# Performance work log

Measured on AMD Instinct MI355X. Metric: run time of the kernel, lower is better.

The kernel has to match this reference:

```python
import jax, jax.numpy as jnp
import numpy as np

N, E, F, H, C = 50000, 800000, 602, 32, 41
BN_EPS = 1e-5


def _mlp(h, Wa, ba, Wb, bb):
    return jax.nn.relu(h @ Wa + ba) @ Wb + bb


def _bn(h, gamma, beta):
    # BatchNorm1d training mode: per-feature batch mean / biased variance
    m = jnp.mean(h, axis=0)
    v = jnp.var(h, axis=0)
    return (h - m) * jax.lax.rsqrt(v + BN_EPS) * gamma + beta


def _gin(x, row, col, Wa, ba, Wb, bb):
    # sum-aggregate neighbor features (SpMM via gather + segment_sum), eps=0
    agg = jax.ops.segment_sum(x[col], row, num_segments=x.shape[0])
    return _mlp(x + agg, Wa, ba, Wb, bb)


def setup_inputs() -> dict:
    key = jax.random.key(0)
    ks = jax.random.split(key, 16)
    s = 0.05
    inp = {
        "x": jax.random.normal(ks[0], (N, F), dtype=jnp.float32),
        "row": jax.random.randint(ks[1], (E,), 0, N),
        "col": jax.random.randint(ks[2], (E,), 0, N),
        # conv1 MLP
        "W1a": jax.random.normal(ks[3], (F, H), dtype=jnp.float32) * s,
        "b1a": jnp.zeros((H,), jnp.float32),
        "W1b": jax.random.normal(ks[4], (H, H), dtype=jnp.float32) * s,
        "b1b": jnp.zeros((H,), jnp.float32),
        "g1": jnp.ones((H,), jnp.float32),
        "be1": jnp.zeros((H,), jnp.float32),
        # conv2 MLP
        "W2a": jax.random.normal(ks[5], (H, H), dtype=jnp.float32) * s,
        "b2a": jnp.zeros((H,), jnp.float32),
        "W2b": jax.random.normal(ks[6], (H, H), dtype=jnp.float32) * s,
        "b2b": jnp.zeros((H,), jnp.float32),
        "g2": jnp.ones((H,), jnp.float32),
        "be2": jnp.zeros((H,), jnp.float32),
        # heads
        "Wf1": jax.random.normal(ks[7], (H, H), dtype=jnp.float32) * s,
        "bf1": jnp.zeros((H,), jnp.float32),
        "Wf2": jax.random.normal(ks[8], (H, C), dtype=jnp.float32) * s,
        "bf2": jnp.zeros((C,), jnp.float32),
    }
    return inp


def reference(x, row, col, W1a, b1a, W1b, b1b, g1, be1,
              W2a, b2a, W2b, b2b, g2, be2, Wf1, bf1, Wf2, bf2):
    h = _bn(_gin(x, row, col, W1a, b1a, W1b, b1b), g1, be1)
    h = _bn(_gin(h, row, col, W2a, b2a, W2b, b2b), g2, be2)
    h = jax.nn.relu(h @ Wf1 + bf1)
    return h @ Wf2 + bf2
```

## Files before the change

### kernel.cpp

```cpp
#include <hip/hip_runtime.h>
#include <hip/hip_bf16.h>

#define N_NODES 50000
#define F_IN    602
#define H_DIM   32
#define C_OUT   41
#define E_EDGES 800000
#define BN_EPS  1e-5f

typedef short bf16x8 __attribute__((ext_vector_type(8)));
typedef float f32x4  __attribute__((ext_vector_type(4)));

__device__ inline unsigned short f2bf(float f) {
  unsigned int u = __builtin_bit_cast(unsigned int, f);
  unsigned int r = (u + 0x7FFFu + ((u >> 16) & 1u)) >> 16;
  return (unsigned short)r;
}

__global__ __launch_bounds__(256) void k_gemm_mfma(
    const float* __restrict__ x, const float* __restrict__ W,
    float* __restrict__ p) {
  __shared__ unsigned short xh[64 * 40], xl[64 * 40];
  __shared__ unsigned short wh[32 * 40], wl[32 * 40];
  const int tid = threadIdx.x;
  const int wv = tid >> 6, ln = tid & 63;
  const int m = ln & 15, q = ln >> 4;
  const int r0 = blockIdx.x * 64;

  const int srow = tid >> 4, ks2 = tid & 15;
  const int wk = tid >> 3, c4 = tid & 7;

  float2 xr[4];
  float4 wr;

  auto prefetch = [&](int k0) {
    #pragma unroll
    for (int pp = 0; pp < 4; pp++) {
      int rr = r0 + srow + 16 * pp;
      int k = k0 + 2 * ks2;
      float2 v = {0.f, 0.f};
      if (rr < N_NODES && k <= F_IN - 2) v = *(const float2*)(x + (size_t)rr * F_IN + k);
      xr[pp] = v;
    }
    {
      int k = k0 + wk;
      float4 v = {0.f, 0.f, 0.f, 0.f};
      if (k < F_IN) v = *(const float4*)(W + (size_t)k * H_DIM + 4 * c4);
      wr = v;
    }
  };

  f32x4 acc0 = {0.f, 0.f, 0.f, 0.f};
  f32x4 acc1 = {0.f, 0.f, 0.f, 0.f};

  prefetch(0);

  unsigned int* xh32 = (unsigned int*)xh;
  unsigned int* xl32 = (unsigned int*)xl;

  for (int ch = 0; ch < 19; ch++) {
    __syncthreads();
    #pragma unroll
    for (int pp = 0; pp < 4; pp++) {
      int row = srow + 16 * pp;
      float2 v = xr[pp];
      unsigned short h0 = f2bf(v.x), h1 = f2bf(v.y);
      float f0 = __builtin_bit_cast(float, (unsigned int)h0 << 16);
      float f1 = __builtin_bit_cast(float, (unsigned int)h1 << 16);
      unsigned short l0 = f2bf(v.x - f0), l1 = f2bf(v.y - f1);
      xh32[row * 20 + ks2] = (unsigned int)h0 | ((unsigned int)h1 << 16);
      xl32[row * 20 + ks2] = (unsigned int)l0 | ((unsigned int)l1 << 16);
    }
    {
      float wf[4] = {wr.x, wr.y, wr.z, wr.w};
      #pragma unroll
      for (int i = 0; i < 4; i++) {
        unsigned short hh = f2bf(wf[i]);
        float fh = __builtin_bit_cast(float, (unsigned int)hh << 16);
        unsigned short ll = f2bf(wf[i] - fh);
        wh[(4 * c4 + i) * 40 + wk] = hh;
        wl[(4 * c4 + i) * 40 + wk] = ll;
      }
    }
    __syncthreads();
    if (ch < 18) prefetch((ch + 1) * 32);

    const int abase = (16 * wv + m) * 40 + q * 8;
    const int bbase = m * 40 + q * 8;
    bf16x8 axh = *(const bf16x8*)&xh[abase];
    bf16x8 axl = *(const bf16x8*)&xl[abase];
    bf16x8 b0h = *(const bf16x8*)&wh[bbase];
    bf16x8 b0l = *(const bf16x8*)&wl[bbase];
    bf16x8 b1h = *(const bf16x8*)&wh[bbase + 16 * 40];
    bf16x8 b1l = *(const bf16x8*)&wl[bbase + 16 * 40];
    acc0 = __builtin_amdgcn_mfma_f32_16x16x32_bf16(axh, b0h, acc0, 0, 0, 0);
    acc1 = __builtin_amdgcn_mfma_f32_16x16x32_bf16(axh, b1h, acc1, 0, 0, 0);
    acc0 = __builtin_amdgcn_mfma_f32_16x16x32_bf16(axl, b0h, acc0, 0, 0, 0);
    acc1 = __builtin_amdgcn_mfma_f32_16x16x32_bf16(axl, b1h, acc1, 0, 0, 0);
    acc0 = __builtin_amdgcn_mfma_f32_16x16x32_bf16(axh, b0l, acc0, 0, 0, 0);
    acc1 = __builtin_amdgcn_mfma_f32_16x16x32_bf16(axh, b1l, acc1, 0, 0, 0);
  }

  #pragma unroll
  for (int reg = 0; reg < 4; reg++) {
    int rowg = r0 + 16 * wv + q * 4 + reg;
    if (rowg < N_NODES) {
      p[(size_t)rowg * H_DIM + m]      = acc0[reg];
      p[(size_t)rowg * H_DIM + m + 16] = acc1[reg];
    }
  }
}

__global__ __launch_bounds__(256) void k_hist(const int* __restrict__ row,
                                              int* __restrict__ deg) {
  int e = blockIdx.x * 256 + threadIdx.x;
  if (e < E_EDGES) atomicAdd(&deg[row[e]], 1);
}

__global__ __launch_bounds__(256) void k_scanA(const int* __restrict__ deg,
                                               int* __restrict__ start,
                                               int* __restrict__ bsum) {
  __shared__ int sc[256];
  int t = threadIdx.x, i = blockIdx.x * 256 + t;
  int v = (i < N_NODES) ? deg[i] : 0;
  sc[t] = v;
  __syncthreads();
  #pragma unroll
  for (int off = 1; off < 256; off <<= 1) {
    int u = (t >= off) ? sc[t - off] : 0;
    __syncthreads();
    sc[t] += u;
    __syncthreads();
  }
  if (i < N_NODES) start[i] = sc[t] - v;
  if (t == 255) bsum[blockIdx.x] = sc[255];
}

__global__ __launch_bounds__(256) void k_scanB(const int* __restrict__ bsum,
                                               int* __restrict__ boff, int nb) {
  __shared__ int sc[256];
  int t = threadIdx.x;
  int v = (t < nb) ? bsum[t] : 0;
  sc[t] = v;
  __syncthreads();
  #pragma unroll
  for (int off = 1; off < 256; off <<= 1) {
    int u = (t >= off) ? sc[t - off] : 0;
    __syncthreads();
    sc[t] += u;
    __syncthreads();
  }
  if (t < nb) boff[t] = sc[t] - v;
}

__global__ __launch_bounds__(256) void k_scanC(int* __restrict__ start,
                                               const int* __restrict__ boff,
                                               int* __restrict__ cursor) {
  int i = blockIdx.x * 256 + threadIdx.x;
  if (i < N_NODES) {
    int s = start[i] + boff[blockIdx.x];
    start[i] = s;
    cursor[i] = s;
  }
  if (i == 0) start[N_NODES] = E_EDGES;
}

__global__ __launch_bounds__(256) void k_fill(const int* __restrict__ row,
                                              const int* __restrict__ col,
                                              int* __restrict__ cursor,
                                              int* __restrict__ ecol) {
  int e = blockIdx.x * 256 + threadIdx.x;
  if (e < E_EDGES) {
    int pos = atomicAdd(&cursor[row[e]], 1);
    ecol[pos] = col[e];
  }
}

__global__ __launch_bounds__(256) void k_gather_mlp(
    const float* __restrict__ p, const float* __restrict__ bagg,
    const int* __restrict__ start, const int* __restrict__ ecol,
    const float* __restrict__ Wm, const float* __restrict__ bm,
    float* __restrict__ hpre, float* __restrict__ stats) {
  __shared__ float as_[64 * 36];
  __shared__ float ws[32 * 36];
  __shared__ float red[512];
  const int tid = threadIdx.x;
  for (int i = tid; i < 1024; i += 256) {
    int k = i >> 5, c = i & 31;
    ws[c * 36 + k] = Wm[(size_t)k * H_DIM + c];
  }
  const int hw = tid >> 5, c = tid & 31;
  const int n0 = blockIdx.x * 64;
  const float bca = bagg[c];
  for (int s = 0; s < 8; s++) {
    int lr = hw * 8 + s;
    int n = n0 + lr;
    float acc = 0.f;
    if (n < N_NODES) {
      acc = p[(size_t)n * H_DIM + c] + bca;
      int i0 = start[n], i1 = start[n + 1];
      int i = i0;
      for (; i + 3 < i1; i += 4) {
        int s0 = ecol[i], s1 = ecol[i + 1], s2 = ecol[i + 2], s3 = ecol[i + 3];
        float v0 = p[(size_t)s0 * H_DIM + c];
        float v1 = p[(size_t)s1 * H_DIM + c];
        float v2 = p[(size_t)s2 * H_DIM + c];
        float v3 = p[(size_t)s3 * H_DIM + c];
        acc += v0; acc += v1; acc += v2; acc += v3;
      }
      for (; i < i1; i++) acc += p[(size_t)ecol[i] * H_DIM + c];
      acc = fmaxf(acc, 0.f);
    }
    as_[lr * 36 + c] = acc;
  }
  __syncthreads();
  const int rg = tid >> 5;
  float4 wc[8];
  #pragma unroll
  for (int qq = 0; qq < 8; qq++) wc[qq] = *(float4*)&ws[c * 36 + qq * 4];
  const float bc = bm[c];
  float lsum = 0.f, lsq = 0.f;
  #pragma unroll
  for (int i = 0; i < 8; i++) {
    int r = rg * 8 + i;
    float a = bc;
    #pragma unroll
    for (int qq = 0; qq < 8; qq++) {
      float4 h4 = *(float4*)&as_[r * 36 + qq * 4];
      a += h4.x * wc[qq].x + h4.y * wc[qq].y + h4.z * wc[qq].z + h4.w * wc[qq].w;
    }
    int gr = n0 + r;
    if (gr < N_NODES) {
      hpre[(size_t)gr * H_DIM + c] = a;
      lsum += a; lsq += a * a;
    }
  }
  __syncthreads();
  red[tid] = lsum; red[256 + tid] = lsq;
  __syncthreads();
  if (tid < 32) {
    float s = 0.f, qv = 0.f;
    #pragma unroll
    for (int g = 0; g < 8; g++) { s += red[g * 32 + tid]; qv += red[256 + g * 32 + tid]; }
    atomicAdd(&stats[tid], s);
    atomicAdd(&stats[32 + tid], qv);
  }
}

__global__ __launch_bounds__(256) void k_zinit(const float* __restrict__ p,
                                               const float* __restrict__ b,
                                               float* __restrict__ z) {
  int i = blockIdx.x * 256 + threadIdx.x;
  if (i < N_NODES * H_DIM) z[i] = p[i] + b[i & 31];
}

__global__ __launch_bounds__(256) void k_scatter(
    const int* __restrict__ row, const int* __restrict__ col,
    const float* __restrict__ p, float* __restrict__ z) {
  long long t = (long long)blockIdx.x * 256 + threadIdx.x;
  int e = (int)(t >> 5);
  int c = (int)(t & 31);
  if (e < E_EDGES) {
    int s = col[e], d = row[e];
    atomicAdd(&z[(size_t)d * H_DIM + c], p[(size_t)s * H_DIM + c]);
  }
}

__global__ __launch_bounds__(256) void k_mlp_stats(
    const float* __restrict__ z, const float* __restrict__ W,
    const float* __restrict__ b, float* __restrict__ hpre,
    float* __restrict__ stats) {
  __shared__ float as_[64 * 36];
  __shared__ float ws[32 * 36];
  __shared__ float red[512];
  const int tid = threadIdx.x;
  for (int i = tid; i < 1024; i += 256) {
    int k = i >> 5, c = i & 31;
    ws[c * 36 + k] = W[(size_t)k * H_DIM + c];
  }
  const int r0 = blockIdx.x * 64;
  for (int i = tid; i < 2048; i += 256) {
    int r = i >> 5, c = i & 31;
    int gr = r0 + r;
    float v = (gr < N_NODES) ? z[(size_t)gr * H_DIM + c] : 0.f;
    as_[r * 36 + c] = fmaxf(v, 0.f);
  }
  __syncthreads();
  const int c = tid & 31, rg = tid >> 5;
  float4 wc[8];
  #pragma unroll
  for (int q = 0; q < 8; q++) wc[q] = *(float4*)&ws[c * 36 + q * 4];
  const float bc = b[c];
  float lsum = 0.f, lsq = 0.f;
  #pragma unroll
  for (int i = 0; i < 8; i++) {
    int r = rg * 8 + i;
    float a = bc;
    #pragma unroll
    for (int q = 0; q < 8; q++) {
      float4 h4 = *(float4*)&as_[r * 36 + q * 4];
      a += h4.x * wc[q].x + h4.y * wc[q].y + h4.z * wc[q].z + h4.w * wc[q].w;
    }
    int gr = r0 + r;
    if (gr < N_NODES) {
      hpre[(size_t)gr * H_DIM + c] = a;
      lsum += a; lsq += a * a;
    }
  }
  __syncthreads();
  red[tid] = lsum; red[256 + tid] = lsq;
  __syncthreads();
  if (tid < 32) {
    float s = 0.f, q = 0.f;
    #pragma unroll
    for (int g = 0; g < 8; g++) { s += red[g * 32 + tid]; q += red[256 + g * 32 + tid]; }
    atomicAdd(&stats[tid], s);
    atomicAdd(&stats[32 + tid], q);
  }
}

__global__ __launch_bounds__(256) void k_gemm32_affine(
    const float* __restrict__ hpre, const float* __restrict__ stats,
    const float* __restrict__ g, const float* __restrict__ be,
    const float* __restrict__ W, float* __restrict__ p) {
  __shared__ float hs[64 * 36];
  __shared__ float ws[32 * 36];
  __shared__ float ssl[64];
  const int tid = threadIdx.x;
  if (tid < 32) {
    float m = stats[tid] * (1.f / N_NODES);
    float v = stats[32 + tid] * (1.f / N_NODES) - m * m;
    float sc = g[tid] * rsqrtf(v + BN_EPS);
    ssl[tid] = sc;
    ssl[32 + tid] = be[tid] - m * sc;
  }
  for (int i = tid; i < 1024; i += 256) {
    int k = i >> 5, c = i & 31;
    ws[c * 36 + k] = W[(size_t)k * H_DIM + c];
  }
  __syncthreads();
  const int r0 = blockIdx.x * 64;
  for (int i = tid; i < 2048; i += 256) {
    int r = i >> 5, c = i & 31;
    int gr = r0 + r;
    float v = (gr < N_NODES) ? hpre[(size_t)gr * H_DIM + c] * ssl[c] + ssl[32 + c] : 0.f;
    hs[r * 36 + c] = v;
  }
  __syncthreads();
  const int c = tid & 31, rg = tid >> 5;
  float4 wc[8];
  #pragma unroll
  for (int q = 0; q < 8; q++) wc[q] = *(float4*)&ws[c * 36 + q * 4];
  #pragma unroll
  for (int i = 0; i < 8; i++) {
    int r = rg * 8 + i;
    float a = 0.f;
    #pragma unroll
    for (int q = 0; q < 8; q++) {
      float4 h4 = *(float4*)&hs[r * 36 + q * 4];
      a += h4.x * wc[q].x + h4.y * wc[q].y + h4.z * wc[q].z + h4.w * wc[q].w;
    }
    int gr = r0 + r;
    if (gr < N_NODES) p[(size_t)gr * H_DIM + c] = a;
  }
}

__global__ __launch_bounds__(256) void k_heads(
    const float* __restrict__ hpre, const float* __restrict__ stats,
    const float* __restrict__ g, const float* __restrict__ be,
    const float* __restrict__ W1, const float* __restrict__ b1,
    const float* __restrict__ W2, const float* __restrict__ b2,
    float* __restrict__ out) {
  __shared__ float hs[64 * 36];
  __shared__ float fs[64 * 36];
  __shared__ float w1[32 * 36];
  __shared__ float w2[41 * 36];
  __shared__ float ssl[64];
  const int tid = threadIdx.x;
  if (tid < 32) {
    float m = stats[tid] * (1.f / N_NODES);
    float v = stats[32 + tid] * (1.f / N_NODES) - m * m;
    float sc = g[tid] * rsqrtf(v + BN_EPS);
    ssl[tid] = sc;
    ssl[32 + tid] = be[tid] - m * sc;
  }
  for (int i = tid; i < 1024; i += 256) {
    int k = i >> 5, c = i & 31;
    w1[c * 36 + k] = W1[(size_t)k * H_DIM + c];
  }
  for (int i = tid; i < 41 * 32; i += 256) {
    int j = i >> 5, k = i & 31;
    w2[j * 36 + k] = W2[(size_t)k * C_OUT + j];
  }
  __syncthreads();
  const int r0 = blockIdx.x * 64;
  for (int i = tid; i < 2048; i += 256) {
    int r = i >> 5, c = i & 31;
    int gr = r0 + r;
    hs[r * 36 + c] = (gr < N_NODES) ? hpre[(size_t)gr * H_DIM + c] * ssl[c] + ssl[32 + c] : 0.f;
  }
  __syncthreads();
  {
    const int c = tid & 31, rg = tid >> 5;
    float4 wc[8];
    #pragma unroll
    for (int q = 0; q < 8; q++) wc[q] = *(float4*)&w1[c * 36 + q * 4];
    const float bc = b1[c];
    #pragma unroll
    for (int i = 0; i < 8; i++) {
      int r = rg * 8 + i;
      float a = bc;
      #pragma unroll
      for (int q = 0; q < 8; q++) {
        float4 h4 = *(float4*)&hs[r * 36 + q * 4];
        a += h4.x * wc[q].x + h4.y * wc[q].y + h4.z * wc[q].z + h4.w * wc[q].w;
      }
      fs[r * 36 + c] = fmaxf(a, 0.f);
    }
  }
  __syncthreads();
  for (int idx = tid; idx < 64 * C_OUT; idx += 256) {
    int r = idx / C_OUT, j = idx - r * C_OUT;
    int gr = r0 + r;
    if (gr < N_NODES) {
      float a = b2[j];
      #pragma unroll
      for (int q = 0; q < 8; q++) {
        float4 f4 = *(float4*)&fs[r * 36 + q * 4];
        float4 w4 = *(float4*)&w2[j * 36 + q * 4];
        a += f4.x * w4.x + f4.y * w4.y + f4.z * w4.z + f4.w * w4.w;
      }
      out[(size_t)gr * C_OUT + j] = a;
    }
  }
}

extern "C" void kernel_launch(void* const* d_in, const int* in_sizes, int n_in,
                              void* d_out, int out_size, void* d_ws, size_t ws_size,
                              hipStream_t stream) {
  const float* x   = (const float*)d_in[0];
  const int* row   = (const int*)d_in[1];
  const int* col   = (const int*)d_in[2];
  const float* W1a = (const float*)d_in[3];
  const float* b1a = (const float*)d_in[4];
  const float* W1b = (const float*)d_in[5];
  const float* b1b = (const float*)d_in[6];
  const float* g1  = (const float*)d_in[7];
  const float* be1 = (const float*)d_in[8];
  const float* W2a = (const float*)d_in[9];
  const float* b2a = (const float*)d_in[10];
  const float* W2b = (const float*)d_in[11];
  const float* b2b = (const float*)d_in[12];
  const float* g2  = (const float*)d_in[13];
  const float* be2 = (const float*)d_in[14];
  const float* Wf1 = (const float*)d_in[15];
  const float* bf1 = (const float*)d_in[16];
  const float* Wf2 = (const float*)d_in[17];
  const float* bf2 = (const float*)d_in[18];
  float* out = (float*)d_out;

  float* ws = (float*)d_ws;
  const size_t NH = (size_t)N_NODES * H_DIM;
  float* pA    = ws;
  float* zB    = ws + NH;
  float* hC    = ws + 2 * NH;
  float* stats = ws + 3 * NH;
  int*   startA = (int*)(ws + 3 * NH + 256);
  int*   cursor = startA + 50016;
  int*   deg    = cursor + 50016;
  int*   ecol   = deg + 50016;
  int*   bsum   = ecol + E_EDGES;
  int*   boff   = bsum + 256;
  const size_t need_bytes = ((3 * NH + 256) + 3 * 50016 + E_EDGES + 512) * 4;
  const bool use_csr = (ws_size >= need_bytes);

  hipMemsetAsync(stats, 0, 128 * sizeof(float), stream);

  const int g64   = (N_NODES + 63) / 64;
  const int gE    = (E_EDGES + 255) / 256;
  const int gN    = (N_NODES + 255) / 256;
  const int gScat = (E_EDGES * 32 + 255) / 256;

  if (use_csr) {
    hipMemsetAsync(deg, 0, 50000 * sizeof(int), stream);
    k_hist <<<gE, 256, 0, stream>>>(row, deg);
    k_scanA<<<gN, 256, 0, stream>>>(deg, startA, bsum);
    k_scanB<<<1, 256, 0, stream>>>(bsum, boff, gN);
    k_scanC<<<gN, 256, 0, stream>>>(startA, boff, cursor);
    k_fill <<<gE, 256, 0, stream>>>(row, col, cursor, ecol);
  }

  k_gemm_mfma<<<g64, 256, 0, stream>>>(x, W1a, pA);
  if (use_csr) {
    k_gather_mlp<<<g64, 256, 0, stream>>>(pA, b1a, startA, ecol, W1b, b1b, hC, stats);
  } else {
    k_zinit<<<g64 * 8, 256, 0, stream>>>(pA, b1a, zB);
    k_scatter<<<gScat, 256, 0, stream>>>(row, col, pA, zB);
    k_mlp_stats<<<g64, 256, 0, stream>>>(zB, W1b, b1b, hC, stats);
  }
  k_gemm32_affine<<<g64, 256, 0, stream>>>(hC, stats, g1, be1, W2a, pA);
  if (use_csr) {
    k_gather_mlp<<<g64, 256, 0, stream>>>(pA, b2a, startA, ecol, W2b, b2b, hC, stats + 64);
  } else {
    k_zinit<<<g64 * 8, 256, 0, stream>>>(pA, b2a, zB);
    k_scatter<<<gScat, 256, 0, stream>>>(row, col, pA, zB);
    k_mlp_stats<<<g64, 256, 0, stream>>>(zB, W2b, b2b, hC, stats + 64);
  }
  k_heads<<<g64, 256, 0, stream>>>(hC, stats + 64, g2, be2, Wf1, bf1, Wf2, bf2, out);
}
```

Baseline: 462.5 us.

## Split gather from MLP and merge the three-pass scan into one block

The fused gather+MLP kernel, which walked 8 nodes serially per half-wave, is replaced by a standalone gather kernel. That kernel gives each node its own 32-lane group and unrolls the neighbour loop by 8 for more memory-level parallelism. The MLP and statistics then run through the existing k_mlp_stats kernel on the aggregated buffer. The three-kernel degree prefix scan becomes a single 1024-thread block that scans 49 elements per thread, cutting launches. The cost is an extra global round trip of the aggregated features per layer, plus a serial, strided single-block scan.

```diff
diff --git a/kernel.cpp b/kernel.cpp
--- a/kernel.cpp
+++ b/kernel.cpp
@@ -117,52 +117,40 @@
   if (e < E_EDGES) atomicAdd(&deg[row[e]], 1);
 }
 
-__global__ __launch_bounds__(256) void k_scanA(const int* __restrict__ deg,
-                                               int* __restrict__ start,
-                                               int* __restrict__ bsum) {
-  __shared__ int sc[256];
-  int t = threadIdx.x, i = blockIdx.x * 256 + t;
-  int v = (i < N_NODES) ? deg[i] : 0;
-  sc[t] = v;
-  __syncthreads();
-  #pragma unroll
-  for (int off = 1; off < 256; off <<= 1) {
+#define SCAN_T 1024
+#define SCAN_PER 49
+__global__ __launch_bounds__(SCAN_T) void k_scan1(
+    const int* __restrict__ deg, int* __restrict__ start,
+    int* __restrict__ cursor) {
+  __shared__ int sc[SCAN_T];
+  const int t = threadIdx.x;
+  const int base = t * SCAN_PER;
+  int lsum = 0;
+  #pragma unroll 7
+  for (int j = 0; j < SCAN_PER; j++) {
+    int idx = base + j;
+    if (idx < N_NODES) lsum += deg[idx];
+  }
+  sc[t] = lsum;
+  __syncthreads();
+  #pragma unroll
+  for (int off = 1; off < SCAN_T; off <<= 1) {
     int u = (t >= off) ? sc[t - off] : 0;
     __syncthreads();
     sc[t] += u;
     __syncthreads();
   }
-  if (i < N_NODES) start[i] = sc[t] - v;
-  if (t == 255) bsum[blockIdx.x] = sc[255];
-}
-
-__global__ __launch_bounds__(256) void k_scanB(const int* __restrict__ bsum,
-                                               int* __restrict__ boff, int nb) {
-  __shared__ int sc[256];
-  int t = threadIdx.x;
-  int v = (t < nb) ? bsum[t] : 0;
-  sc[t] = v;
-  __syncthreads();
-  #pragma unroll
-  for (int off = 1; off < 256; off <<= 1) {
-    int u = (t >= off) ? sc[t - off] : 0;
-    __syncthreads();
-    sc[t] += u;
-    __syncthreads();
-  }
-  if (t < nb) boff[t] = sc[t] - v;
-}
-
-__global__ __launch_bounds__(256) void k_scanC(int* __restrict__ start,
-                                               const int* __restrict__ boff,
-                                               int* __restrict__ cursor) {
-  int i = blockIdx.x * 256 + threadIdx.x;
-  if (i < N_NODES) {
-    int s = start[i] + boff[blockIdx.x];
-    start[i] = s;
-    cursor[i] = s;
-  }
-  if (i == 0) start[N_NODES] = E_EDGES;
+  int run = sc[t] - lsum;
+  #pragma unroll 7
+  for (int j = 0; j < SCAN_PER; j++) {
+    int idx = base + j;
+    if (idx < N_NODES) {
+      start[idx] = run;
+      cursor[idx] = run;
+      run += deg[idx];
+    }
+  }
+  if (t == 0) start[N_NODES] = E_EDGES;
 }
 
 __global__ __launch_bounds__(256) void k_fill(const int* __restrict__ row,
@@ -176,75 +164,40 @@
   }
 }
 
-__global__ __launch_bounds__(256) void k_gather_mlp(
-    const float* __restrict__ p, const float* __restrict__ bagg,
+__global__ __launch_bounds__(256) void k_gather(
+    const float* __restrict__ p, const float* __restrict__ b,
     const int* __restrict__ start, const int* __restrict__ ecol,
-    const float* __restrict__ Wm, const float* __restrict__ bm,
-    float* __restrict__ hpre, float* __restrict__ stats) {
-  __shared__ float as_[64 * 36];
-  __shared__ float ws[32 * 36];
-  __shared__ float red[512];
-  const int tid = threadIdx.x;
-  for (int i = tid; i < 1024; i += 256) {
-    int k = i >> 5, c = i & 31;
-    ws[c * 36 + k] = Wm[(size_t)k * H_DIM + c];
-  }
-  const int hw = tid >> 5, c = tid & 31;
-  const int n0 = blockIdx.x * 64;
-  const float bca = bagg[c];
-  for (int s = 0; s < 8; s++) {
-    int lr = hw * 8 + s;
-    int n = n0 + lr;
-    float acc = 0.f;
-    if (n < N_NODES) {
-      acc = p[(size_t)n * H_DIM + c] + bca;
-      int i0 = start[n], i1 = start[n + 1];
-      int i = i0;
-      for (; i + 3 < i1; i += 4) {
-        int s0 = ecol[i], s1 = ecol[i + 1], s2 = ecol[i + 2], s3 = ecol[i + 3];
-        float v0 = p[(size_t)s0 * H_DIM + c];
-        float v1 = p[(size_t)s1 * H_DIM + c];
-        float v2 = p[(size_t)s2 * H_DIM + c];
-        float v3 = p[(size_t)s3 * H_DIM + c];
-        acc += v0; acc += v1; acc += v2; acc += v3;
-      }
-      for (; i < i1; i++) acc += p[(size_t)ecol[i] * H_DIM + c];
-      acc = fmaxf(acc, 0.f);
-    }
-    as_[lr * 36 + c] = acc;
-  }
-  __syncthreads();
-  const int rg = tid >> 5;
-  float4 wc[8];
-  #pragma unroll
-  for (int qq = 0; qq < 8; qq++) wc[qq] = *(float4*)&ws[c * 36 + qq * 4];
-  const float bc = bm[c];
-  float lsum = 0.f, lsq = 0.f;
-  #pragma unroll
-  for (int i = 0; i < 8; i++) {
-    int r = rg * 8 + i;
-    float a = bc;
-    #pragma unroll
-    for (int qq = 0; qq < 8; qq++) {
-      float4 h4 = *(float4*)&as_[r * 36 + qq * 4];
-      a += h4.x * wc[qq].x + h4.y * wc[qq].y + h4.z * wc[qq].z + h4.w * wc[qq].w;
-    }
-    int gr = n0 + r;
-    if (gr < N_NODES) {
-      hpre[(size_t)gr * H_DIM + c] = a;
-      lsum += a; lsq += a * a;
-    }
-  }
-  __syncthreads();
-  red[tid] = lsum; red[256 + tid] = lsq;
-  __syncthreads();
-  if (tid < 32) {
-    float s = 0.f, qv = 0.f;
-    #pragma unroll
-    for (int g = 0; g < 8; g++) { s += red[g * 32 + tid]; qv += red[256 + g * 32 + tid]; }
-    atomicAdd(&stats[tid], s);
-    atomicAdd(&stats[32 + tid], qv);
-  }
+    float* __restrict__ z) {
+  int hw = (blockIdx.x * 256 + threadIdx.x) >> 5;
+  int c = threadIdx.x & 31;
+  if (hw >= N_NODES) return;
+  int s = start[hw], e = start[hw + 1];
+  float acc = p[(size_t)hw * H_DIM + c] + b[c];
+  int i = s;
+  for (; i + 7 < e; i += 8) {
+    int s0 = ecol[i],     s1 = ecol[i + 1], s2 = ecol[i + 2], s3 = ecol[i + 3];
+    int s4 = ecol[i + 4], s5 = ecol[i + 5], s6 = ecol[i + 6], s7 = ecol[i + 7];
+    float v0 = p[(size_t)s0 * H_DIM + c];
+    float v1 = p[(size_t)s1 * H_DIM + c];
+    float v2 = p[(size_t)s2 * H_DIM + c];
+    float v3 = p[(size_t)s3 * H_DIM + c];
+    float v4 = p[(size_t)s4 * H_DIM + c];
+    float v5 = p[(size_t)s5 * H_DIM + c];
+    float v6 = p[(size_t)s6 * H_DIM + c];
+    float v7 = p[(size_t)s7 * H_DIM + c];
+    acc += v0; acc += v1; acc += v2; acc += v3;
+    acc += v4; acc += v5; acc += v6; acc += v7;
+  }
+  for (; i + 3 < e; i += 4) {
+    int s0 = ecol[i], s1 = ecol[i + 1], s2 = ecol[i + 2], s3 = ecol[i + 3];
+    float v0 = p[(size_t)s0 * H_DIM + c];
+    float v1 = p[(size_t)s1 * H_DIM + c];
+    float v2 = p[(size_t)s2 * H_DIM + c];
+    float v3 = p[(size_t)s3 * H_DIM + c];
+    acc += v0; acc += v1; acc += v2; acc += v3;
+  }
+  for (; i < e; i++) acc += p[(size_t)ecol[i] * H_DIM + c];
+  z[(size_t)hw * H_DIM + c] = acc;
 }
 
 __global__ __launch_bounds__(256) void k_zinit(const float* __restrict__ p,
@@ -469,8 +422,6 @@
   int*   cursor = startA + 50016;
   int*   deg    = cursor + 50016;
   int*   ecol   = deg + 50016;
-  int*   bsum   = ecol + E_EDGES;
-  int*   boff   = bsum + 256;
   const size_t need_bytes = ((3 * NH + 256) + 3 * 50016 + E_EDGES + 512) * 4;
   const bool use_csr = (ws_size >= need_bytes);
 
@@ -478,33 +429,31 @@
 
   const int g64   = (N_NODES + 63) / 64;
   const int gE    = (E_EDGES + 255) / 256;
-  const int gN    = (N_NODES + 255) / 256;
+  const int gHW   = (N_NODES * 32 + 255) / 256;
   const int gScat = (E_EDGES * 32 + 255) / 256;
 
   if (use_csr) {
     hipMemsetAsync(deg, 0, 50000 * sizeof(int), stream);
     k_hist <<<gE, 256, 0, stream>>>(row, deg);
-    k_scanA<<<gN, 256, 0, stream>>>(deg, startA, bsum);
-    k_scanB<<<1, 256, 0, stream>>>(bsum, boff, gN);
-    k_scanC<<<gN, 256, 0, stream>>>(startA, boff, cursor);
+    k_scan1<<<1, SCAN_T, 0, stream>>>(deg, startA, cursor);
     k_fill <<<gE, 256, 0, stream>>>(row, col, cursor, ecol);
   }
 
   k_gemm_mfma<<<g64, 256, 0, stream>>>(x, W1a, pA);
   if (use_csr) {
-    k_gather_mlp<<<g64, 256, 0, stream>>>(pA, b1a, startA, ecol, W1b, b1b, hC, stats);
+    k_gather<<<gHW, 256, 0, stream>>>(pA, b1a, startA, ecol, zB);
   } else {
     k_zinit<<<g64 * 8, 256, 0, stream>>>(pA, b1a, zB);
     k_scatter<<<gScat, 256, 0, stream>>>(row, col, pA, zB);
-    k_mlp_stats<<<g64, 256, 0, stream>>>(zB, W1b, b1b, hC, stats);
-  }
+  }
+  k_mlp_stats<<<g64, 256, 0, stream>>>(zB, W1b, b1b, hC, stats);
   k_gemm32_affine<<<g64, 256, 0, stream>>>(hC, stats, g1, be1, W2a, pA);
   if (use_csr) {
-    k_gather_mlp<<<g64, 256, 0, stream>>>(pA, b2a, startA, ecol, W2b, b2b, hC, stats + 64);
+    k_gather<<<gHW, 256, 0, stream>>>(pA, b2a, startA, ecol, zB);
   } else {
     k_zinit<<<g64 * 8, 256, 0, stream>>>(pA, b2a, zB);
     k_scatter<<<gScat, 256, 0, stream>>>(row, col, pA, zB);
-    k_mlp_stats<<<g64, 256, 0, stream>>>(zB, W2b, b2b, hC, stats + 64);
-  }
+  }
+  k_mlp_stats<<<g64, 256, 0, stream>>>(zB, W2b, b2b, hC, stats + 64);
   k_heads<<<g64, 256, 0, stream>>>(hC, stats + 64, g2, be2, Wf1, bf1, Wf2, bf2, out);
 }
```

Result: slower. 556.5 us (+20.3%).
